# Performance work log

Measured on AMD Instinct MI355X. Metric: run time of the kernel, lower is better.

Reference implementation:

```python
import jax, jax.numpy as jnp
import numpy as np

# Module hyperparameters (BNMorph.__init__ defaults + KITTI resolution)
B, H, W = 8, 320, 1024
SEARCH_W = 7      # serachWidth
SEARCH_H = 3      # searchHeight
SPARSITY_RAD = 2
SENSE_R = 20
PIX_DW = 24.0     # pixel_distance_weight
ALPHA_DW = 0.7    # alpha_distance_weight
PIX_MUL_DW = 1.9  # pixel_mulline_distance_weight
ALPHA_PAD = 1.6   # alpha_padding
EDGE_DENSITY = 0.02


def _make_offsets():
    # Exactly mirrors BNMorph.__init__ buffer construction.
    rs = np.arange(-SEARCH_W, SEARCH_W + 1)
    cs = np.arange(-SEARCH_H, SEARCH_H + 1)
    xx, yy = np.meshgrid(rs, cs)
    xx = xx.flatten(); yy = yy.flatten()
    idx = np.argsort(xx ** 2 + yy ** 2)
    xx = xx[idx]; yy = yy[idx]
    ss = np.arange(-SPARSITY_RAD, SPARSITY_RAD + 1)
    sxx, syy = np.meshgrid(ss, ss)
    sxx = sxx.flatten(); syy = syy.flatten()
    cspan = np.arange(-SENSE_R, SENSE_R + 1)
    cxx, cyy = np.meshgrid(cspan, cspan)
    cxx = cxx.flatten(); cyy = cyy.flatten()
    ci = np.argsort(cxx ** 2 + cyy ** 2)
    cxx = cxx[ci]; cyy = cyy[ci]
    f32 = lambda a: jnp.asarray(a, dtype=jnp.float32)
    return f32(xx), f32(yy), f32(sxx), f32(syy), f32(cxx), f32(cyy)


def setup_inputs() -> dict:
    key = jax.random.key(0)
    k1, k2 = jax.random.split(key)
    binMapsrc = (jax.random.uniform(k1, (B, 1, H, W)) < EDGE_DENSITY).astype(jnp.float32)
    binMapdst = (jax.random.uniform(k2, (B, 1, H, W)) < EDGE_DENSITY).astype(jnp.float32)
    xx, yy, sxx, syy, cxx, cyy = _make_offsets()
    return {"binMapsrc": binMapsrc, "binMapdst": binMapdst,
            "xx": xx, "yy": yy, "sxx": sxx, "syy": syy, "cxx": cxx, "cyy": cyy}


def _forward(binMapsrc, binMapdst, xx, yy, sxx, syy, cxx, cyy):
    src = binMapsrc[:, 0] > 0.5  # [B,H,W] bool
    dst = binMapdst[:, 0] > 0.5
    b, h, w = src.shape

    # ---- 1. sparsity filtering of src edge points ----
    # keep an active pixel iff no active pixel precedes it (raster order)
    # inside the sparsity window -> approximates greedy sparsification.
    sdx = sxx.astype(jnp.int32); sdy = syy.astype(jnp.int32)
    prec = ((sdy < 0) | ((sdy == 0) & (sdx < 0))).astype(jnp.float32)
    Ps = jnp.pad(src.astype(jnp.float32),
                 ((0, 0), (SPARSITY_RAD, SPARSITY_RAD), (SPARSITY_RAD, SPARSITY_RAD)))

    def sp_step(acc, off):
        dx, dy, wk = off
        sl = jax.lax.dynamic_slice(Ps, (0, SPARSITY_RAD + dy, SPARSITY_RAD + dx), (b, h, w))
        return acc + sl * wk, None

    acc, _ = jax.lax.scan(sp_step, jnp.zeros((b, h, w), jnp.float32), (sdx, sdy, prec))
    kept = src & (acc < 0.5)

    # ---- 2. windowed nearest-correspondence search in dst ----
    # offsets (xx,yy) are pre-sorted by distance, so the first hit is nearest.
    qdx = xx.astype(jnp.int32); qdy = yy.astype(jnp.int32)
    Pd = jnp.pad(dst, ((0, 0), (SEARCH_H, SEARCH_H), (SEARCH_W, SEARCH_W)))

    def m_step(carry, off):
        found, vx, vy = carry
        dx, dy, dxf, dyf = off
        sl = jax.lax.dynamic_slice(Pd, (0, SEARCH_H + dy, SEARCH_W + dx), (b, h, w))
        hit = sl & kept & (~found)
        vx = jnp.where(hit, dxf, vx)
        vy = jnp.where(hit, dyf, vy)
        return (found | hit, vx, vy), None

    init = (jnp.zeros((b, h, w), bool),
            jnp.zeros((b, h, w), jnp.float32),
            jnp.zeros((b, h, w), jnp.float32))
    (found, vx, vy), _ = jax.lax.scan(m_step, init, (qdx, qdy, xx, yy))

    # ---- 3. distance-weighted morph field (splat = depthwise conv) ----
    d = jnp.sqrt(cxx ** 2 + cyy ** 2)
    wts = ALPHA_DW * jnp.exp(-d * PIX_MUL_DW / PIX_DW)
    R = SENSE_R
    K = jnp.zeros((2 * R + 1, 2 * R + 1), jnp.float32)
    K = K.at[cyy.astype(jnp.int32) + R, cxx.astype(jnp.int32) + R].set(wts)

    m = found.astype(jnp.float32)
    inp = jnp.stack([m, m * vx, m * vy], axis=1)        # [B,3,H,W]
    ker = jnp.tile(K[None, None], (3, 1, 1, 1))          # [3,1,41,41]
    out = jax.lax.conv_general_dilated(
        inp, ker, (1, 1), ((R, R), (R, R)),
        dimension_numbers=("NCHW", "OIHW", "NCHW"), feature_group_count=3)
    den = out[:, 0] + ALPHA_PAD
    dispx = out[:, 1] / den
    dispy = out[:, 2] / den

    ygrid, xgrid = jnp.meshgrid(jnp.arange(h, dtype=jnp.float32),
                                jnp.arange(w, dtype=jnp.float32), indexing="ij")
    morphedx = xgrid + dispx
    morphedy = ygrid + dispy
    orgpts_x = xgrid * m
    orgpts_y = ygrid * m
    correspts_x = (xgrid + vx) * m
    correspts_y = (ygrid + vy) * m
    return morphedx, morphedy, orgpts_x, orgpts_y, correspts_x, correspts_y


def reference(binMapsrc, binMapdst, xx, yy, sxx, syy, cxx, cyy):
    return _forward(binMapsrc, binMapdst, xx, yy, sxx, syy, cxx, cyy)
```

## Files before the change

kernel.cpp:

```cpp
#include <hip/hip_runtime.h>


#define BB 8
#define HH 320
#define WW 1024
#define N_PIX (BB*HH*WW)
#define WPI (HH*(WW/32))
#define RR 20
#define TLW 64
#define TLH 32
#define TXN (WW/TLW)
#define TYN (HH/TLH)
#define TPB (TXN*TYN)
#define N_TILES (BB*TPB)
#define NQ 105
#define CAP_MAX 512
#define PACK_OFF 16384
#define WTABN (4*42*48)
#define WTAB_OFF (PACK_OFF + 2*BB*WPI*4)
#define LISTS_OFF (WTAB_OFF + WTABN*4)

typedef unsigned long long u64;
typedef float v2f __attribute__((ext_vector_type(2)));

__global__ __launch_bounds__(256) void pack_zero(
    const float* __restrict__ src, const float* __restrict__ dst,
    unsigned* __restrict__ packed, int* __restrict__ cnt,
    float* __restrict__ wtab_g)
{
    int t = threadIdx.x;
    int i = blockIdx.x * 256 + t;
    if (i < N_TILES) cnt[i] = 0;
    if (i < WTABN) {
        int rot = i / (42 * 48);
        int rem = i - rot * (42 * 48);
        int row = rem / 48, c = rem - row * 48;
        int pc = c + rot;
        float v = 0.0f;
        if (row <= 40 && pc >= 4 && pc <= 44) {
            int dxv = pc - 24, dyv = row - 20;
            float d = sqrtf((float)(dxv * dxv + dyv * dyv));
            v = 0.7f * expf((-d * 1.9f) / 24.0f);
        }
        wtab_g[i] = v;
    }
    const float4* p = (i < (N_PIX >> 2)) ? (const float4*)src + i
                                         : (const float4*)dst + (i - (N_PIX >> 2));
    float4 v = *p;
    unsigned nib = (v.x > 0.5f ? 1u : 0u) | (v.y > 0.5f ? 2u : 0u)
                 | (v.z > 0.5f ? 4u : 0u) | (v.w > 0.5f ? 8u : 0u);
    unsigned val = nib << ((t & 7) * 4);
    val |= __shfl_xor(val, 1);
    val |= __shfl_xor(val, 2);
    val |= __shfl_xor(val, 4);
    if ((t & 7) == 0) packed[i >> 3] = val;
}

__global__ __launch_bounds__(256) void build_points(
    const unsigned* __restrict__ packed,
    const float* __restrict__ xx, const float* __restrict__ yy,
    int* __restrict__ cnt, unsigned* __restrict__ lists, int cap)
{
    __shared__ unsigned sS[4][32];
    __shared__ unsigned sD[8][32];
    __shared__ unsigned sPtXY[128];
    __shared__ unsigned sPk[128];
    __shared__ unsigned sPairs[512];
    __shared__ int prank[NQ], sdxv[NQ], sdyv[NQ];
    __shared__ int lcnt[2];

    int t  = threadIdx.x;
    int y0 = blockIdx.x * 2;
    int b  = blockIdx.y;
    const unsigned* psrc = packed + (size_t)b * WPI;
    const unsigned* pdst = packed + (size_t)(BB + b) * WPI;

    {
        int r = t >> 5, w = t & 31;
        int y2 = y0 - 3 + r;
        sD[r][w] = (y2 >= 0 && y2 < HH) ? pdst[(y2 << 5) + w] : 0u;
        if (t < 128) {
            int y3 = y0 - 2 + (t >> 5);
            sS[t >> 5][w] = (y3 >= 0) ? psrc[(y3 << 5) + w] : 0u;
        }
    }
    if (t < NQ) {
        int dx = (int)xx[t], dy = (int)yy[t];
        sdxv[t] = dx; sdyv[t] = dy;
        prank[(dy + 3) * 15 + (dx + 7)] = t;
    }
    if (t < 2) lcnt[t] = 0;
    __syncthreads();

    if (t < 64) {
        int r = t >> 5, w = t & 31;
        unsigned C = sS[r + 2][w];
        unsigned kept = 0;
        if (C) {
            #define EXT5(row) ( (u64)((w ? (row)[w-1] : 0u) >> 30) \
                              | ((u64)(row)[w] << 2) \
                              | ((u64)((w < 31 ? (row)[w+1] : 0u) & 3u) << 34) )
            u64 a = EXT5(sS[r]) | EXT5(sS[r + 1]);
            u64 or5 = a | (a >> 1) | (a >> 2) | (a >> 3) | (a >> 4);
            u64 e2 = EXT5(sS[r + 2]);
            u64 or2 = e2 | (e2 >> 1);
            kept = C & ~(unsigned)(or5 | or2);
        }
        unsigned found = 0;
        if (kept) {
            u64 dil = 0;
            #pragma unroll
            for (int rr = 0; rr < 7; ++rr) {
                const unsigned* row = sD[r + rr];
                unsigned L = w ? row[w-1] : 0u;
                unsigned R = (w < 31) ? row[w+1] : 0u;
                dil |= (u64)(L >> 25) | ((u64)row[w] << 7) | ((u64)(R & 0x7Fu) << 39);
            }
            u64 a2 = dil | (dil >> 1);
            u64 b2 = a2 | (a2 >> 2);
            u64 c2 = b2 | (b2 >> 4);
            u64 o15 = c2 | (c2 >> 7);
            found = kept & (unsigned)o15;
        }
        int nf = __popc(found);
        if (nf) {
            int base = atomicAdd(&lcnt[0], nf);
            unsigned fi = found;
            while (fi) {
                int bit = __builtin_ctz(fi); fi &= fi - 1;
                if (base < 128) sPtXY[base] = (unsigned)((r << 10) | (w << 5) | bit);
                ++base;
            }
        }
    }
    __syncthreads();
    int nPts = lcnt[0]; if (nPts > 128) nPts = 128;

    if (t < nPts) {
        unsigned e = sPtXY[t];
        int r = e >> 10, x = (int)(e & 1023u);
        int y = y0 + r;
        int x7 = x - 7;
        int j = x7 >> 5;
        int sh = x7 & 31;
        u64 lo = 0, hi = 0;
        #pragma unroll
        for (int rr = 0; rr < 7; ++rr) {
            const unsigned* row = sD[r + rr];
            unsigned W0 = (j >= 0) ? row[j] : 0u;
            unsigned W1 = (j + 1 < 32) ? row[j + 1] : 0u;
            u64 win = (((u64)W0 | ((u64)W1 << 32)) >> sh) & 0x7FFFull;
            if (rr < 4) lo |= win << (15 * rr);
            else        hi |= win << (15 * (rr - 4));
        }
        int minr = NQ - 1;
        while (lo) { int bb2 = __builtin_ctzll(lo); lo &= lo - 1; int rk = prank[bb2];      if (rk < minr) minr = rk; }
        while (hi) { int bb2 = __builtin_ctzll(hi); hi &= hi - 1; int rk = prank[60 + bb2]; if (rk < minr) minr = rk; }
        int vx = sdxv[minr], vy = sdyv[minr];

        sPk[t] = (unsigned)x | ((unsigned)y << 10)
               | ((unsigned)(vx + 7) << 19) | ((unsigned)(vy + 3) << 23);

        int txl = x - RR; txl = (txl < 0 ? 0 : txl) >> 6;
        int txh = x + RR; txh = (txh > WW - 1 ? WW - 1 : txh) >> 6;
        int tyl = y - RR; tyl = (tyl < 0 ? 0 : tyl) >> 5;
        int tyh = y + RR; tyh = (tyh > HH - 1 ? HH - 1 : tyh) >> 5;
        int np = (txh - txl + 1) * (tyh - tyl + 1);
        int base = atomicAdd(&lcnt[1], np);
        for (int ty = tyl; ty <= tyh; ++ty)
            for (int tx = txl; tx <= txh; ++tx) {
                if (base < 512)
                    sPairs[base] = ((unsigned)t << 16) | (unsigned)(b * TPB + ty * TXN + tx);
                ++base;
            }
    }
    __syncthreads();
    int nPairs = lcnt[1]; if (nPairs > 512) nPairs = 512;

    for (int jj = t; jj < nPairs; jj += 256) {
        unsigned pr = sPairs[jj];
        int tile = (int)(pr & 0xFFFFu);
        int i    = (int)(pr >> 16);
        int pos = atomicAdd(&cnt[tile], 1);
        if (pos < cap) lists[(size_t)tile * cap + pos] = sPk[i];
    }
}

__global__ __launch_bounds__(256, 4) void splat_finalize(
    const int* __restrict__ cnt, const unsigned* __restrict__ lists,
    const float* __restrict__ wtab_g,
    float* __restrict__ out, int cap)
{
    __shared__ __align__(16) float wtab[WTABN];
    __shared__ __align__(16) unsigned sWav[4][264];
    int t = threadIdx.x;
    int lane = t & 63, w = t >> 6;

    for (int i = t; i < WTABN / 4; i += 256)
        ((float4*)wtab)[i] = ((const float4*)wtab_g)[i];

    int txT = blockIdx.x, tyT = blockIdx.y, b = blockIdx.z;
    int tile = b * TPB + tyT * TXN + txT;
    const unsigned* lp = lists + (size_t)tile * cap;
    int n = cnt[tile]; if (n > cap) n = cap;

    int wy0 = tyT * TLH + w * 8;
    int cw = 0;
    for (int base = 0; base < n; base += 64) {
        int i = base + lane;
        unsigned pk = 0xFFFFFFFFu;
        if (i < n) pk = lp[i];
        int py = (int)((pk >> 10) & 511u);
        bool pass = (i < n) & (py >= wy0 - 20) & (py <= wy0 + 27);
        u64 m = __ballot(pass);
        if (pass) {
            int idx = __popcll(m & ((1ull << lane) - 1ull));
            if (cw + idx < 256) sWav[w][cw + idx] = pk;
        }
        cw += __popcll(m);
    }
    if (cw > 256) cw = 256;
    int c4 = (cw + 3) & ~3;
    if (lane < c4 - cw) sWav[w][cw + lane] = 0xFFFFFFFFu;
    __syncthreads();

    int x0  = txT * TLW + (t & 15) * 4;
    int y0t = tyT * TLH + (t >> 4) * 2;

    v2f a0p[2][2] = {};
    v2f av[2][4]  = {};

    for (int p = 0; p < c4; p += 4) {
        uint4 P = *(const uint4*)&sWav[w][p];
        #pragma unroll
        for (int k = 0; k < 4; ++k) {
            int spk = __builtin_amdgcn_readfirstlane(
                (int)(k == 0 ? P.x : k == 1 ? P.y : k == 2 ? P.z : P.w));
            int pxp21 = (spk & 1023) + 21;
            int pyp20 = ((spk >> 10) & 511) + 20;
            float pvx = (float)(((spk >> 19) & 15) - 7);
            float pvy = (float)(((spk >> 23) & 7) - 3);
            v2f vv = {pvx, pvy};

            int coff = pxp21 - x0;
            coff = coff < 0 ? 0 : (coff > 45 ? 45 : coff);
            int rot = coff & 3;
            int cb  = rot * (42 * 48) + (coff & ~3);
            #pragma unroll
            for (int ry = 0; ry < 2; ++ry) {
                int dyr = pyp20 - (y0t + ry);
                int rowi = ((unsigned)dyr > 40u) ? 41 : dyr;
                float4 wv = *(const float4*)&wtab[cb + rowi * 48];
                a0p[ry][0] += (v2f){wv.w, wv.z};
                a0p[ry][1] += (v2f){wv.y, wv.x};
                av[ry][0] += wv.w * vv;
                av[ry][1] += wv.z * vv;
                av[ry][2] += wv.y * vv;
                av[ry][3] += wv.x * vv;
            }
        }
    }

    size_t bbase = (size_t)b * HH * WW;
    float4 z4 = {0.f, 0.f, 0.f, 0.f};
    #pragma unroll
    for (int ry = 0; ry < 2; ++ry) {
        int y = y0t + ry;
        size_t idx = bbase + (size_t)y * WW + x0;
        float d0 = a0p[ry][0].x + 1.6f, d1 = a0p[ry][0].y + 1.6f;
        float d2 = a0p[ry][1].x + 1.6f, d3 = a0p[ry][1].y + 1.6f;
        float4 ox = { (float)x0     + av[ry][0].x / d0, (float)(x0+1) + av[ry][1].x / d1,
                      (float)(x0+2) + av[ry][2].x / d2, (float)(x0+3) + av[ry][3].x / d3 };
        float4 oy = { (float)y + av[ry][0].y / d0, (float)y + av[ry][1].y / d1,
                      (float)y + av[ry][2].y / d2, (float)y + av[ry][3].y / d3 };
        *reinterpret_cast<float4*>(out + idx)                     = ox;
        *reinterpret_cast<float4*>(out + (size_t)N_PIX + idx)     = oy;
        *reinterpret_cast<float4*>(out + 2 * (size_t)N_PIX + idx) = z4;
        *reinterpret_cast<float4*>(out + 3 * (size_t)N_PIX + idx) = z4;
        *reinterpret_cast<float4*>(out + 4 * (size_t)N_PIX + idx) = z4;
        *reinterpret_cast<float4*>(out + 5 * (size_t)N_PIX + idx) = z4;
    }
    __syncthreads();

    int tx0 = txT * TLW, ty0 = tyT * TLH;
    for (int i = t; i < n; i += 256) {
        unsigned pk = lp[i];
        int px = (int)(pk & 1023u);
        int py = (int)((pk >> 10) & 511u);
        if (px >= tx0 && px < tx0 + TLW && py >= ty0 && py < ty0 + TLH) {
            int vx = (int)((pk >> 19) & 15u) - 7;
            int vy = (int)((pk >> 23) & 7u) - 3;
            size_t idx = bbase + (size_t)py * WW + px;
            out[2 * (size_t)N_PIX + idx] = (float)px;
            out[3 * (size_t)N_PIX + idx] = (float)py;
            out[4 * (size_t)N_PIX + idx] = (float)(px + vx);
            out[5 * (size_t)N_PIX + idx] = (float)(py + vy);
        }
    }
}

extern "C" void kernel_launch(void* const* d_in, const int* in_sizes, int n_in,
                              void* d_out, int out_size, void* d_ws, size_t ws_size,
                              hipStream_t stream) {
    const float* src = (const float*)d_in[0];
    const float* dst = (const float*)d_in[1];
    const float* xx  = (const float*)d_in[2];
    const float* yy  = (const float*)d_in[3];
    float* out = (float*)d_out;

    int*      cnt    = (int*)d_ws;
    unsigned* packed = (unsigned*)((char*)d_ws + PACK_OFF);
    float*    wtab_g = (float*)((char*)d_ws + WTAB_OFF);
    unsigned* lists  = (unsigned*)((char*)d_ws + LISTS_OFF);

    int cap = CAP_MAX;
    size_t need = (size_t)LISTS_OFF + (size_t)N_TILES * cap * sizeof(unsigned);
    if (ws_size < need) {
        long avail = ((long)ws_size - LISTS_OFF) / ((long)N_TILES * 4);
        cap = avail < 1 ? 1 : (avail > CAP_MAX ? CAP_MAX : (int)avail);
    }

    pack_zero<<<(2 * N_PIX / 4) / 256, 256, 0, stream>>>(src, dst, packed, cnt, wtab_g);

    dim3 g1(HH / 2, BB);
    build_points<<<g1, 256, 0, stream>>>(packed, xx, yy, cnt, lists, cap);

    dim3 g2(TXN, TYN, BB);
    splat_finalize<<<g2, 256, 0, stream>>>(cnt, lists, wtab_g, out, cap);
}
```

Measured before the change: 138.4 us.

## Fuse point detection into per-tile splat kernel, removing global tile lists

```diff
diff --git a/kernel.cpp b/kernel.cpp
--- a/kernel.cpp
+++ b/kernel.cpp
@@ -11,26 +11,20 @@
 #define TLH 32
 #define TXN (WW/TLW)
 #define TYN (HH/TLH)
-#define TPB (TXN*TYN)
-#define N_TILES (BB*TPB)
 #define NQ 105
-#define CAP_MAX 512
-#define PACK_OFF 16384
+#define CAP 192
 #define WTABN (4*42*48)
-#define WTAB_OFF (PACK_OFF + 2*BB*WPI*4)
-#define LISTS_OFF (WTAB_OFF + WTABN*4)
+#define WTAB_OFF (2*BB*WPI*4)
 
 typedef unsigned long long u64;
 typedef float v2f __attribute__((ext_vector_type(2)));
 
 __global__ __launch_bounds__(256) void pack_zero(
     const float* __restrict__ src, const float* __restrict__ dst,
-    unsigned* __restrict__ packed, int* __restrict__ cnt,
-    float* __restrict__ wtab_g)
+    unsigned* __restrict__ packed, float* __restrict__ wtab_g)
 {
     int t = threadIdx.x;
     int i = blockIdx.x * 256 + t;
-    if (i < N_TILES) cnt[i] = 0;
     if (i < WTABN) {
         int rot = i / (42 * 48);
         int rem = i - rot * (42 * 48);
@@ -56,182 +50,128 @@
     if ((t & 7) == 0) packed[i >> 3] = val;
 }
 
-__global__ __launch_bounds__(256) void build_points(
+__global__ __launch_bounds__(256, 4) void fused_morph(
     const unsigned* __restrict__ packed,
     const float* __restrict__ xx, const float* __restrict__ yy,
-    int* __restrict__ cnt, unsigned* __restrict__ lists, int cap)
+    const float* __restrict__ wtab_g,
+    float* __restrict__ out)
 {
-    __shared__ unsigned sS[4][32];
-    __shared__ unsigned sD[8][32];
-    __shared__ unsigned sPtXY[128];
-    __shared__ unsigned sPk[128];
-    __shared__ unsigned sPairs[512];
-    __shared__ int prank[NQ], sdxv[NQ], sdyv[NQ];
-    __shared__ int lcnt[2];
-
-    int t  = threadIdx.x;
-    int y0 = blockIdx.x * 2;
-    int b  = blockIdx.y;
+    __shared__ __align__(16) float wtab[WTABN];
+    __shared__ unsigned sSrc[74][6];
+    __shared__ unsigned sDst[78][6];
+    __shared__ __align__(16) unsigned sPt[CAP];
+    __shared__ int prank[NQ];
+    __shared__ unsigned char sVB[TLH * TLW];
+    __shared__ int lcnt;
+
+    int t = threadIdx.x;
+    int txT = blockIdx.x, tyT = blockIdx.y, b = blockIdx.z;
+    int tx0 = txT * TLW, ty0 = tyT * TLH;
+    int wb0 = (tx0 >> 5) - 1;
     const unsigned* psrc = packed + (size_t)b * WPI;
     const unsigned* pdst = packed + (size_t)(BB + b) * WPI;
 
-    {
-        int r = t >> 5, w = t & 31;
-        int y2 = y0 - 3 + r;
-        sD[r][w] = (y2 >= 0 && y2 < HH) ? pdst[(y2 << 5) + w] : 0u;
-        if (t < 128) {
-            int y3 = y0 - 2 + (t >> 5);
-            sS[t >> 5][w] = (y3 >= 0) ? psrc[(y3 << 5) + w] : 0u;
-        }
-    }
+    for (int i = t; i < WTABN / 4; i += 256)
+        ((float4*)wtab)[i] = ((const float4*)wtab_g)[i];
+    for (int i = t; i < 74 * 4; i += 256) {
+        int r = i >> 2, w = (i & 3) + 1;
+        int gy = ty0 - 22 + r, gw = wb0 + (w - 1);
+        sSrc[r][w] = (gy >= 0 && gy < HH && gw >= 0 && gw < 32) ? psrc[(gy << 5) + gw] : 0u;
+    }
+    for (int i = t; i < 78 * 4; i += 256) {
+        int r = i >> 2, w = (i & 3) + 1;
+        int gy = ty0 - 23 + r, gw = wb0 + (w - 1);
+        sDst[r][w] = (gy >= 0 && gy < HH && gw >= 0 && gw < 32) ? pdst[(gy << 5) + gw] : 0u;
+    }
+    if (t < 78) { sDst[t][0] = 0; sDst[t][5] = 0; if (t < 74) { sSrc[t][0] = 0; sSrc[t][5] = 0; } }
     if (t < NQ) {
         int dx = (int)xx[t], dy = (int)yy[t];
-        sdxv[t] = dx; sdyv[t] = dy;
-        prank[(dy + 3) * 15 + (dx + 7)] = t;
-    }
-    if (t < 2) lcnt[t] = 0;
+        prank[(dy + 3) * 15 + (dx + 7)] = (t << 8) | ((dx + 7) << 4) | (dy + 3);
+    }
+    ((unsigned*)sVB)[t] = 0; ((unsigned*)sVB)[t + 256] = 0;
+    if (t == 0) lcnt = 0;
     __syncthreads();
 
-    if (t < 64) {
-        int r = t >> 5, w = t & 31;
-        unsigned C = sS[r + 2][w];
-        unsigned kept = 0;
+    for (int task = t; task < 288; task += 256) {
+        int cr = task >> 2, w = (task & 3) + 1;
+        unsigned C = sSrc[cr + 2][w];
+        unsigned found = 0;
         if (C) {
-            #define EXT5(row) ( (u64)((w ? (row)[w-1] : 0u) >> 30) \
+            #define EXT5(row) ( (u64)((row)[w-1] >> 30) \
                               | ((u64)(row)[w] << 2) \
-                              | ((u64)((w < 31 ? (row)[w+1] : 0u) & 3u) << 34) )
-            u64 a = EXT5(sS[r]) | EXT5(sS[r + 1]);
+                              | ((u64)((row)[w+1] & 3u) << 34) )
+            u64 a = EXT5(sSrc[cr]) | EXT5(sSrc[cr + 1]);
             u64 or5 = a | (a >> 1) | (a >> 2) | (a >> 3) | (a >> 4);
-            u64 e2 = EXT5(sS[r + 2]);
-            u64 or2 = e2 | (e2 >> 1);
-            kept = C & ~(unsigned)(or5 | or2);
-        }
-        unsigned found = 0;
-        if (kept) {
-            u64 dil = 0;
-            #pragma unroll
-            for (int rr = 0; rr < 7; ++rr) {
-                const unsigned* row = sD[r + rr];
-                unsigned L = w ? row[w-1] : 0u;
-                unsigned R = (w < 31) ? row[w+1] : 0u;
-                dil |= (u64)(L >> 25) | ((u64)row[w] << 7) | ((u64)(R & 0x7Fu) << 39);
+            u64 e2 = EXT5(sSrc[cr + 2]);
+            unsigned kept = C & ~(unsigned)(or5 | e2 | (e2 >> 1));
+            if (kept) {
+                u64 dil = 0;
+                #pragma unroll
+                for (int rr = 0; rr < 7; ++rr) {
+                    const unsigned* row = sDst[cr + rr];
+                    dil |= (u64)(row[w-1] >> 25) | ((u64)row[w] << 7)
+                         | ((u64)(row[w+1] & 0x7Fu) << 39);
+                }
+                u64 a2 = dil | (dil >> 1);
+                u64 b2 = a2 | (a2 >> 2);
+                u64 c2 = b2 | (b2 >> 4);
+                u64 o15 = c2 | (c2 >> 7);
+                found = kept & (unsigned)o15;
             }
-            u64 a2 = dil | (dil >> 1);
-            u64 b2 = a2 | (a2 >> 2);
-            u64 c2 = b2 | (b2 >> 4);
-            u64 o15 = c2 | (c2 >> 7);
-            found = kept & (unsigned)o15;
-        }
-        int nf = __popc(found);
-        if (nf) {
-            int base = atomicAdd(&lcnt[0], nf);
+        }
+        if (w == 1) found &= 0xFFFFF000u;
+        if (w == 4) found &= 0x000FFFFFu;
+        if (found) {
+            int nf = __popc(found);
+            int base = atomicAdd(&lcnt, nf);
             unsigned fi = found;
             while (fi) {
                 int bit = __builtin_ctz(fi); fi &= fi - 1;
-                if (base < 128) sPtXY[base] = (unsigned)((r << 10) | (w << 5) | bit);
+                int px = tx0 - 32 + ((w - 1) << 5) + bit;
+                if (base < CAP) sPt[base] = (unsigned)((cr << 10) | px);
                 ++base;
             }
         }
     }
     __syncthreads();
-    int nPts = lcnt[0]; if (nPts > 128) nPts = 128;
+    int nPts = lcnt; if (nPts > CAP) nPts = CAP;
+    int n4 = (nPts + 3) & ~3;
 
     if (t < nPts) {
-        unsigned e = sPtXY[t];
-        int r = e >> 10, x = (int)(e & 1023u);
-        int y = y0 + r;
-        int x7 = x - 7;
-        int j = x7 >> 5;
-        int sh = x7 & 31;
+        unsigned e = sPt[t];
+        int cr = (int)(e >> 10), px = (int)(e & 1023u);
+        int q = px - tx0 + 25;
+        int widx = 1 + (q >> 5), sh = q & 31;
         u64 lo = 0, hi = 0;
         #pragma unroll
         for (int rr = 0; rr < 7; ++rr) {
-            const unsigned* row = sD[r + rr];
-            unsigned W0 = (j >= 0) ? row[j] : 0u;
-            unsigned W1 = (j + 1 < 32) ? row[j + 1] : 0u;
-            u64 win = (((u64)W0 | ((u64)W1 << 32)) >> sh) & 0x7FFFull;
+            const unsigned* row = sDst[cr + rr];
+            u64 win = (((u64)row[widx] | ((u64)row[widx + 1] << 32)) >> sh) & 0x7FFFull;
             if (rr < 4) lo |= win << (15 * rr);
             else        hi |= win << (15 * (rr - 4));
         }
-        int minr = NQ - 1;
-        while (lo) { int bb2 = __builtin_ctzll(lo); lo &= lo - 1; int rk = prank[bb2];      if (rk < minr) minr = rk; }
-        while (hi) { int bb2 = __builtin_ctzll(hi); hi &= hi - 1; int rk = prank[60 + bb2]; if (rk < minr) minr = rk; }
-        int vx = sdxv[minr], vy = sdyv[minr];
-
-        sPk[t] = (unsigned)x | ((unsigned)y << 10)
-               | ((unsigned)(vx + 7) << 19) | ((unsigned)(vy + 3) << 23);
-
-        int txl = x - RR; txl = (txl < 0 ? 0 : txl) >> 6;
-        int txh = x + RR; txh = (txh > WW - 1 ? WW - 1 : txh) >> 6;
-        int tyl = y - RR; tyl = (tyl < 0 ? 0 : tyl) >> 5;
-        int tyh = y + RR; tyh = (tyh > HH - 1 ? HH - 1 : tyh) >> 5;
-        int np = (txh - txl + 1) * (tyh - tyl + 1);
-        int base = atomicAdd(&lcnt[1], np);
-        for (int ty = tyl; ty <= tyh; ++ty)
-            for (int tx = txl; tx <= txh; ++tx) {
-                if (base < 512)
-                    sPairs[base] = ((unsigned)t << 16) | (unsigned)(b * TPB + ty * TXN + tx);
-                ++base;
-            }
-    }
+        int minv = 0x7FFFFFFF;
+        while (lo) { int bb2 = __builtin_ctzll(lo); lo &= lo - 1; int rv = prank[bb2];      if (rv < minv) minv = rv; }
+        while (hi) { int bb2 = __builtin_ctzll(hi); hi &= hi - 1; int rv = prank[60 + bb2]; if (rv < minv) minv = rv; }
+        int vxp7 = (minv >> 4) & 15, vyp3 = minv & 15;
+        int py = ty0 - 20 + cr;
+        sPt[t] = (unsigned)px | ((unsigned)py << 10)
+               | ((unsigned)vxp7 << 19) | ((unsigned)vyp3 << 23);
+        if (px >= tx0 && px < tx0 + TLW && cr >= 20 && cr < 20 + TLH)
+            sVB[(cr - 20) * TLW + (px - tx0)] =
+                (unsigned char)(0x80 | vxp7 | (vyp3 << 4));
+    }
+    if (t < n4 - nPts) sPt[nPts + t] = 0xFFFFFFFFu;
     __syncthreads();
-    int nPairs = lcnt[1]; if (nPairs > 512) nPairs = 512;
-
-    for (int jj = t; jj < nPairs; jj += 256) {
-        unsigned pr = sPairs[jj];
-        int tile = (int)(pr & 0xFFFFu);
-        int i    = (int)(pr >> 16);
-        int pos = atomicAdd(&cnt[tile], 1);
-        if (pos < cap) lists[(size_t)tile * cap + pos] = sPk[i];
-    }
-}
-
-__global__ __launch_bounds__(256, 4) void splat_finalize(
-    const int* __restrict__ cnt, const unsigned* __restrict__ lists,
-    const float* __restrict__ wtab_g,
-    float* __restrict__ out, int cap)
-{
-    __shared__ __align__(16) float wtab[WTABN];
-    __shared__ __align__(16) unsigned sWav[4][264];
-    int t = threadIdx.x;
-    int lane = t & 63, w = t >> 6;
-
-    for (int i = t; i < WTABN / 4; i += 256)
-        ((float4*)wtab)[i] = ((const float4*)wtab_g)[i];
-
-    int txT = blockIdx.x, tyT = blockIdx.y, b = blockIdx.z;
-    int tile = b * TPB + tyT * TXN + txT;
-    const unsigned* lp = lists + (size_t)tile * cap;
-    int n = cnt[tile]; if (n > cap) n = cap;
-
-    int wy0 = tyT * TLH + w * 8;
-    int cw = 0;
-    for (int base = 0; base < n; base += 64) {
-        int i = base + lane;
-        unsigned pk = 0xFFFFFFFFu;
-        if (i < n) pk = lp[i];
-        int py = (int)((pk >> 10) & 511u);
-        bool pass = (i < n) & (py >= wy0 - 20) & (py <= wy0 + 27);
-        u64 m = __ballot(pass);
-        if (pass) {
-            int idx = __popcll(m & ((1ull << lane) - 1ull));
-            if (cw + idx < 256) sWav[w][cw + idx] = pk;
-        }
-        cw += __popcll(m);
-    }
-    if (cw > 256) cw = 256;
-    int c4 = (cw + 3) & ~3;
-    if (lane < c4 - cw) sWav[w][cw + lane] = 0xFFFFFFFFu;
-    __syncthreads();
-
-    int x0  = txT * TLW + (t & 15) * 4;
-    int y0t = tyT * TLH + (t >> 4) * 2;
+
+    int x0q = tx0 + (t & 15) * 4;
+    int y0t = ty0 + (t >> 4) * 2;
 
     v2f a0p[2][2] = {};
     v2f av[2][4]  = {};
 
-    for (int p = 0; p < c4; p += 4) {
-        uint4 P = *(const uint4*)&sWav[w][p];
+    for (int p = 0; p < n4; p += 4) {
+        uint4 P = *(const uint4*)&sPt[p];
         #pragma unroll
         for (int k = 0; k < 4; ++k) {
             int spk = __builtin_amdgcn_readfirstlane(
@@ -242,7 +182,7 @@
             float pvy = (float)(((spk >> 23) & 7) - 3);
             v2f vv = {pvx, pvy};
 
-            int coff = pxp21 - x0;
+            int coff = pxp21 - x0q;
             coff = coff < 0 ? 0 : (coff > 45 ? 45 : coff);
             int rot = coff & 3;
             int cb  = rot * (42 * 48) + (coff & ~3);
@@ -262,40 +202,39 @@
     }
 
     size_t bbase = (size_t)b * HH * WW;
-    float4 z4 = {0.f, 0.f, 0.f, 0.f};
+    int lx = x0q - tx0;
     #pragma unroll
     for (int ry = 0; ry < 2; ++ry) {
         int y = y0t + ry;
-        size_t idx = bbase + (size_t)y * WW + x0;
+        int ly = y - ty0;
+        unsigned vb4 = *(const unsigned*)&sVB[ly * TLW + lx];
+        size_t idx = bbase + (size_t)y * WW + x0q;
         float d0 = a0p[ry][0].x + 1.6f, d1 = a0p[ry][0].y + 1.6f;
         float d2 = a0p[ry][1].x + 1.6f, d3 = a0p[ry][1].y + 1.6f;
-        float4 ox = { (float)x0     + av[ry][0].x / d0, (float)(x0+1) + av[ry][1].x / d1,
-                      (float)(x0+2) + av[ry][2].x / d2, (float)(x0+3) + av[ry][3].x / d3 };
+        float4 ox = { (float)x0q     + av[ry][0].x / d0, (float)(x0q+1) + av[ry][1].x / d1,
+                      (float)(x0q+2) + av[ry][2].x / d2, (float)(x0q+3) + av[ry][3].x / d3 };
         float4 oy = { (float)y + av[ry][0].y / d0, (float)y + av[ry][1].y / d1,
                       (float)y + av[ry][2].y / d2, (float)y + av[ry][3].y / d3 };
+        float4 o2, o3, o4, o5;
+        float* po2 = &o2.x; float* po3 = &o3.x; float* po4 = &o4.x; float* po5 = &o5.x;
+        #pragma unroll
+        for (int jj = 0; jj < 4; ++jj) {
+            unsigned by = (vb4 >> (8 * jj)) & 255u;
+            float fm  = (float)(by >> 7);
+            float fvx = (float)((int)(by & 15u) - 7);
+            float fvy = (float)((int)((by >> 4) & 7u) - 3);
+            float fx  = (float)(x0q + jj);
+            po2[jj] = fx * fm;
+            po3[jj] = (float)y * fm;
+            po4[jj] = (fx + fvx) * fm;
+            po5[jj] = ((float)y + fvy) * fm;
+        }
         *reinterpret_cast<float4*>(out + idx)                     = ox;
         *reinterpret_cast<float4*>(out + (size_t)N_PIX + idx)     = oy;
-        *reinterpret_cast<float4*>(out + 2 * (size_t)N_PIX + idx) = z4;
-        *reinterpret_cast<float4*>(out + 3 * (size_t)N_PIX + idx) = z4;
-        *reinterpret_cast<float4*>(out + 4 * (size_t)N_PIX + idx) = z4;
-        *reinterpret_cast<float4*>(out + 5 * (size_t)N_PIX + idx) = z4;
-    }
-    __syncthreads();
-
-    int tx0 = txT * TLW, ty0 = tyT * TLH;
-    for (int i = t; i < n; i += 256) {
-        unsigned pk = lp[i];
-        int px = (int)(pk & 1023u);
-        int py = (int)((pk >> 10) & 511u);
-        if (px >= tx0 && px < tx0 + TLW && py >= ty0 && py < ty0 + TLH) {
-            int vx = (int)((pk >> 19) & 15u) - 7;
-            int vy = (int)((pk >> 23) & 7u) - 3;
-            size_t idx = bbase + (size_t)py * WW + px;
-            out[2 * (size_t)N_PIX + idx] = (float)px;
-            out[3 * (size_t)N_PIX + idx] = (float)py;
-            out[4 * (size_t)N_PIX + idx] = (float)(px + vx);
-            out[5 * (size_t)N_PIX + idx] = (float)(py + vy);
-        }
+        *reinterpret_cast<float4*>(out + 2 * (size_t)N_PIX + idx) = o2;
+        *reinterpret_cast<float4*>(out + 3 * (size_t)N_PIX + idx) = o3;
+        *reinterpret_cast<float4*>(out + 4 * (size_t)N_PIX + idx) = o4;
+        *reinterpret_cast<float4*>(out + 5 * (size_t)N_PIX + idx) = o5;
     }
 }
 
@@ -308,23 +247,11 @@
     const float* yy  = (const float*)d_in[3];
     float* out = (float*)d_out;
 
-    int*      cnt    = (int*)d_ws;
-    unsigned* packed = (unsigned*)((char*)d_ws + PACK_OFF);
+    unsigned* packed = (unsigned*)d_ws;
     float*    wtab_g = (float*)((char*)d_ws + WTAB_OFF);
-    unsigned* lists  = (unsigned*)((char*)d_ws + LISTS_OFF);
-
-    int cap = CAP_MAX;
-    size_t need = (size_t)LISTS_OFF + (size_t)N_TILES * cap * sizeof(unsigned);
-    if (ws_size < need) {
-        long avail = ((long)ws_size - LISTS_OFF) / ((long)N_TILES * 4);
-        cap = avail < 1 ? 1 : (avail > CAP_MAX ? CAP_MAX : (int)avail);
-    }
-
-    pack_zero<<<(2 * N_PIX / 4) / 256, 256, 0, stream>>>(src, dst, packed, cnt, wtab_g);
-
-    dim3 g1(HH / 2, BB);
-    build_points<<<g1, 256, 0, stream>>>(packed, xx, yy, cnt, lists, cap);
+
+    pack_zero<<<(2 * N_PIX / 4) / 256, 256, 0, stream>>>(src, dst, packed, wtab_g);
 
     dim3 g2(TXN, TYN, BB);
-    splat_finalize<<<g2, 256, 0, stream>>>(cnt, lists, wtab_g, out, cap);
+    fused_morph<<<g2, 256, 0, stream>>>(packed, xx, yy, wtab_g, out);
 }
```

After: 140.1 us. No clear change (+1.2%).
